# Kernel tuning notes

Measured on AMD Instinct MI355X. Metric: run time of the kernel, lower is better.

Reference implementation:

```python
import jax, jax.numpy as jnp
import numpy as np

SCALE = 1.0 / np.sqrt(128.0)  # 1/sqrt(head_size)
NEG = -1000000000.0


def setup_inputs() -> dict:
    key = jax.random.key(0)
    k1, k2, k3, k4 = jax.random.split(key, 4)
    B, H, S, D = 2, 16, 2048, 128
    q = jax.random.normal(k1, (B, H, S, D), dtype=jnp.float32)
    k = jax.random.normal(k2, (B, H, S, D), dtype=jnp.float32)
    v = jax.random.normal(k3, (B, H, S, D), dtype=jnp.float32)
    mask = jax.random.randint(k4, (B, S), 0, 2, dtype=jnp.int32)
    return {"q": q, "k": k, "v": v, "mask": mask}


def reference(q, k, v, mask):
    # scores: [B, H, Sq, Sk]
    scores = jnp.einsum("bhqd,bhkd->bhqk", q, k) * SCALE
    m = mask[:, None, None, :]  # [B,1,1,Sk], broadcast over heads and queries
    scores = jnp.where(m == 0, NEG, scores)
    weights = jax.nn.softmax(scores, axis=-1)
    out = jnp.einsum("bhqk,bhkd->bhqd", weights, v)
    return out
```

## Files before the change

kernel.cpp:

```cpp
#include <hip/hip_runtime.h>
#include <hip/hip_bf16.h>

typedef __attribute__((ext_vector_type(8))) short short8;
typedef __attribute__((ext_vector_type(4))) short short4v;
typedef __attribute__((ext_vector_type(4))) float floatx4;

#define NB 2
#define NH 16
#define NBH 32
#define SS 2048
#define DD 128
#define BQ 128
#define BK 32
#define KTILES (SS / BK)
#define SCALE 0.08838834764831845f
#define LOG2E 1.4426950408889634f
#define MAXB 12.0f
#define MASKED_BIAS -100000.0f

#define WC_VM4 0x0F74
#define WC_VM0 0x0F70
#define WC_ALL0 0x0070

__device__ __forceinline__ short f2bf(float f) {
  union { float f; unsigned u; } x; x.f = f;
  return (short)((x.u + 0x7FFFu + ((x.u >> 16) & 1u)) >> 16);
}

__device__ __forceinline__ void pack8(short8* dst, float a, float b, float c, float d,
                                      float e, float f, float g, float h) {
  union { __hip_bfloat162 h2[4]; short8 v; } u;
  u.h2[0] = __float22bfloat162_rn(make_float2(a, b));
  u.h2[1] = __float22bfloat162_rn(make_float2(c, d));
  u.h2[2] = __float22bfloat162_rn(make_float2(e, f));
  u.h2[3] = __float22bfloat162_rn(make_float2(g, h));
  *dst = u.v;
}

__device__ __forceinline__ void gload_lds16(const short* g, short* l) {
  __builtin_amdgcn_global_load_lds(
      (const __attribute__((address_space(1))) void*)(g),
      (__attribute__((address_space(3))) void*)(l), 16, 0, 0);
}

__global__ __launch_bounds__(256) void prep_kernel(const float* __restrict__ k,
                                                   const float* __restrict__ v,
                                                   short* __restrict__ kbf,
                                                   short* __restrict__ vtg) {
  __shared__ __align__(16) short Ts[DD * 64];
  const int kb = blockIdx.x, bh = blockIdx.y;
  const int tid = threadIdx.x;
  const size_t base = (size_t)bh * SS * DD + (size_t)(kb * 64) * DD;
  const float* kr = k + base;
  const float* vr = v + base;
  short* kw = kbf + base;

#pragma unroll
  for (int c = 0; c < 8; ++c) {
    int fi = c * 256 + tid;
    float4 a = ((const float4*)kr)[fi];
    short4v o;
    o[0] = f2bf(a.x); o[1] = f2bf(a.y); o[2] = f2bf(a.z); o[3] = f2bf(a.w);
    *(short4v*)(kw + (size_t)fi * 4) = o;
  }

  const int kg = tid & 15;
  const int dg0 = tid >> 4;
#pragma unroll
  for (int c = 0; c < 2; ++c) {
    int dg = dg0 + 16 * c;
    float rr[4][4];
#pragma unroll
    for (int r = 0; r < 4; ++r) {
      float4 a = ((const float4*)vr)[(kg * 4 + r) * 32 + dg];
      rr[r][0] = a.x; rr[r][1] = a.y; rr[r][2] = a.z; rr[r][3] = a.w;
    }
#pragma unroll
    for (int j = 0; j < 4; ++j) {
      int d = dg * 4 + j;
      short4v t;
      t[0] = f2bf(rr[0][j]); t[1] = f2bf(rr[1][j]);
      t[2] = f2bf(rr[2][j]); t[3] = f2bf(rr[3][j]);
      int si = d * 64 + (((kg * 8) ^ ((d & 15) << 3)) >> 1);
      *(short4v*)&Ts[si] = t;
    }
  }
  __syncthreads();

#pragma unroll
  for (int s = 0; s < 4; ++s) {
    int d = s * 32 + (tid >> 3);
    int c = tid & 7, kt2 = c >> 2, g = c & 3;
    int x = (d & 15) << 3;
    short4v lo = *(short4v*)&Ts[d * 64 + ((((kt2 * 8 + g) * 8) ^ x) >> 1)];
    short4v hi = *(short4v*)&Ts[d * 64 + ((((kt2 * 8 + g + 4) * 8) ^ x) >> 1)];
    short8 o;
#pragma unroll
    for (int r = 0; r < 4; ++r) { o[r] = lo[r]; o[4 + r] = hi[r]; }
    *(short8*)(vtg + ((size_t)(bh * DD + d)) * SS + (kb * 2 + kt2) * 32 + g * 8) = o;
  }
}

__global__ __launch_bounds__(256, 2) void fa_kernel(
    const float* __restrict__ q, const short* __restrict__ kbf,
    const short* __restrict__ vtg, const int* __restrict__ mask,
    float* __restrict__ out) {
  __shared__ __align__(16) short Ks[4][BK * DD];
  __shared__ __align__(16) short Vt[4][DD * BK];
  __shared__ float Bias[SS];

  const int tid = threadIdx.x;
  const int wave = tid >> 6;
  const int lane = tid & 63;
  const int l16 = lane & 15;
  const int quad = lane >> 4;

  const int lid = blockIdx.y * 16 + blockIdx.x;
  const int vid = (lid & 7) * 64 + (lid >> 3);
  const int bh = vid >> 4;
  const int q0 = (vid & 15) * BQ;
  const int b = bh >> 4;
  const int kt0off = ((bh >> 1) & 1) << 5;

  const size_t base = (size_t)bh * SS * DD;
  const float* qg = q + base;
  const short* kg = kbf + base;
  const short* vgb = vtg + (size_t)bh * DD * SS;
  const int* mg = mask + b * SS;
  const float c1 = SCALE * LOG2E, c2 = MAXB * LOG2E;

  short8 qf[2][4];
#pragma unroll
  for (int t = 0; t < 2; ++t) {
    const float* qp = qg + (size_t)(q0 + wave * 32 + t * 16 + l16) * DD;
#pragma unroll
    for (int dc = 0; dc < 4; ++dc) {
      float4 a = *(const float4*)(qp + dc * 32 + quad * 8);
      float4 bb = *(const float4*)(qp + dc * 32 + quad * 8 + 4);
      short8 tt;
      tt[0] = f2bf(a.x); tt[1] = f2bf(a.y); tt[2] = f2bf(a.z); tt[3] = f2bf(a.w);
      tt[4] = f2bf(bb.x); tt[5] = f2bf(bb.y); tt[6] = f2bf(bb.z); tt[7] = f2bf(bb.w);
      qf[t][dc] = tt;
    }
  }

  {
    int i0 = tid * 8;
    int4 m0 = *(const int4*)(mg + i0);
    int4 m1 = *(const int4*)(mg + i0 + 4);
    float4 f0, f1;
    f0.x = m0.x ? -c2 : MASKED_BIAS; f0.y = m0.y ? -c2 : MASKED_BIAS;
    f0.z = m0.z ? -c2 : MASKED_BIAS; f0.w = m0.w ? -c2 : MASKED_BIAS;
    f1.x = m1.x ? -c2 : MASKED_BIAS; f1.y = m1.y ? -c2 : MASKED_BIAS;
    f1.z = m1.z ? -c2 : MASKED_BIAS; f1.w = m1.w ? -c2 : MASKED_BIAS;
    *(float4*)&Bias[i0] = f0;
    *(float4*)&Bias[i0 + 4] = f1;
  }

  floatx4 Oacc[2][8];
#pragma unroll
  for (int t = 0; t < 2; ++t)
#pragma unroll
    for (int f = 0; f < 8; ++f) Oacc[t][f] = (floatx4){0.f, 0.f, 0.f, 0.f};
  float l_acc[2] = {0.f, 0.f};

  const short* kpg[2];
  const short* vpg[2];
  int kls[2], vls[2];
#pragma unroll
  for (int i = 0; i < 2; ++i) {
    int c = wave * 2 + i;
    int krow = c * 4 + (lane >> 4);
    kpg[i] = kg + (size_t)krow * DD + (((lane & 15) ^ (krow & 7)) * 8);
    int d = c * 16 + (lane >> 2);
    vpg[i] = vgb + (size_t)d * SS + (((lane & 3) ^ ((lane >> 3) & 3)) * 8);
    kls[i] = c * 512;
    vls[i] = c * 512;
  }

  int koff[2];
#pragma unroll
  for (int nt = 0; nt < 2; ++nt) koff[nt] = (nt * 16 + l16) * DD;
  const int ksw = l16 & 7;
  const int voff = l16 * 32 + ((quad ^ ((l16 >> 1) & 3)) * 8);

#pragma unroll
  for (int tt = 0; tt < 3; ++tt) {
    const int ktp = (kt0off + tt) & (KTILES - 1);
    const size_t kadv = (size_t)ktp * (BK * DD);
    const int vadv = ktp * BK;
#pragma unroll
    for (int i = 0; i < 2; ++i) {
      gload_lds16(kpg[i] + kadv, &Ks[tt][kls[i]]);
      gload_lds16(vpg[i] + vadv, &Vt[tt][vls[i]]);
    }
  }
  __builtin_amdgcn_s_waitcnt(WC_ALL0);
  __builtin_amdgcn_s_barrier();

  floatx4 sacc[2][2];
#pragma unroll
  for (int t = 0; t < 2; ++t)
#pragma unroll
    for (int nt = 0; nt < 2; ++nt) sacc[t][nt] = (floatx4){0.f, 0.f, 0.f, 0.f};
  {
    const short* ksb = &Ks[0][0];
    __builtin_amdgcn_s_setprio(1);
#pragma unroll
    for (int nt = 0; nt < 2; ++nt)
#pragma unroll
      for (int dc = 0; dc < 4; ++dc) {
        short8 kf = *(const short8*)(ksb + koff[nt] + (((dc * 4 + quad) ^ ksw) * 8));
        sacc[0][nt] = __builtin_amdgcn_mfma_f32_16x16x32_bf16(kf, qf[0][dc], sacc[0][nt], 0, 0, 0);
        sacc[1][nt] = __builtin_amdgcn_mfma_f32_16x16x32_bf16(kf, qf[1][dc], sacc[1][nt], 0, 0, 0);
      }
    __builtin_amdgcn_s_setprio(0);
  }

#pragma unroll 1
  for (int i = 0; i < KTILES - 1; ++i) {
    const int kt = (i + kt0off) & (KTILES - 1);
    if (i + 2 < KTILES) __builtin_amdgcn_s_waitcnt(WC_VM4);
    else                __builtin_amdgcn_s_waitcnt(WC_VM0);
    __builtin_amdgcn_s_barrier();

    if (i + 3 < KTILES) {
      const int ktp = (kt + 3) & (KTILES - 1);
      const int ib = (i + 3) & 3;
      const size_t kadv = (size_t)ktp * (BK * DD);
      const int vadv = ktp * BK;
#pragma unroll
      for (int c2 = 0; c2 < 2; ++c2) {
        gload_lds16(kpg[c2] + kadv, &Ks[ib][kls[c2]]);
        gload_lds16(vpg[c2] + vadv, &Vt[ib][vls[c2]]);
      }
    }

    float4 bb0 = *(const float4*)&Bias[kt * 32 + quad * 4];
    float4 bb1 = *(const float4*)&Bias[kt * 32 + 16 + quad * 4];

    short8 pb[2];
#pragma unroll
    for (int t = 0; t < 2; ++t) {
      float e0 = __builtin_amdgcn_exp2f(fmaf(sacc[t][0][0], c1, bb0.x));
      float e1 = __builtin_amdgcn_exp2f(fmaf(sacc[t][0][1], c1, bb0.y));
      float e2 = __builtin_amdgcn_exp2f(fmaf(sacc[t][0][2], c1, bb0.z));
      float e3 = __builtin_amdgcn_exp2f(fmaf(sacc[t][0][3], c1, bb0.w));
      float g0 = __builtin_amdgcn_exp2f(fmaf(sacc[t][1][0], c1, bb1.x));
      float g1 = __builtin_amdgcn_exp2f(fmaf(sacc[t][1][1], c1, bb1.y));
      float g2 = __builtin_amdgcn_exp2f(fmaf(sacc[t][1][2], c1, bb1.z));
      float g3 = __builtin_amdgcn_exp2f(fmaf(sacc[t][1][3], c1, bb1.w));
      l_acc[t] += ((e0 + e1) + (e2 + e3)) + ((g0 + g1) + (g2 + g3));
      pack8(&pb[t], e0, e1, e2, e3, g0, g1, g2, g3);
    }

    {
      const short* ksb = &Ks[(i + 1) & 3][0];
#pragma unroll
      for (int t = 0; t < 2; ++t)
#pragma unroll
        for (int nt = 0; nt < 2; ++nt) sacc[t][nt] = (floatx4){0.f, 0.f, 0.f, 0.f};
      __builtin_amdgcn_s_setprio(1);
#pragma unroll
      for (int nt = 0; nt < 2; ++nt)
#pragma unroll
        for (int dc = 0; dc < 4; ++dc) {
          short8 kf = *(const short8*)(ksb + koff[nt] + (((dc * 4 + quad) ^ ksw) * 8));
          sacc[0][nt] = __builtin_amdgcn_mfma_f32_16x16x32_bf16(kf, qf[0][dc], sacc[0][nt], 0, 0, 0);
          sacc[1][nt] = __builtin_amdgcn_mfma_f32_16x16x32_bf16(kf, qf[1][dc], sacc[1][nt], 0, 0, 0);
        }
      __builtin_amdgcn_s_setprio(0);
    }

    {
      const short* vsb = &Vt[i & 3][0];
      __builtin_amdgcn_s_setprio(1);
#pragma unroll
      for (int f = 0; f < 8; ++f) {
        short8 vv = *(const short8*)(vsb + f * 512 + voff);
        Oacc[0][f] = __builtin_amdgcn_mfma_f32_16x16x32_bf16(vv, pb[0], Oacc[0][f], 0, 0, 0);
        Oacc[1][f] = __builtin_amdgcn_mfma_f32_16x16x32_bf16(vv, pb[1], Oacc[1][f], 0, 0, 0);
      }
      __builtin_amdgcn_s_setprio(0);
    }
  }

  {
    const int kt = (KTILES - 1 + kt0off) & (KTILES - 1);
    float4 bb0 = *(const float4*)&Bias[kt * 32 + quad * 4];
    float4 bb1 = *(const float4*)&Bias[kt * 32 + 16 + quad * 4];
    short8 pb[2];
#pragma unroll
    for (int t = 0; t < 2; ++t) {
      float e0 = __builtin_amdgcn_exp2f(fmaf(sacc[t][0][0], c1, bb0.x));
      float e1 = __builtin_amdgcn_exp2f(fmaf(sacc[t][0][1], c1, bb0.y));
      float e2 = __builtin_amdgcn_exp2f(fmaf(sacc[t][0][2], c1, bb0.z));
      float e3 = __builtin_amdgcn_exp2f(fmaf(sacc[t][0][3], c1, bb0.w));
      float g0 = __builtin_amdgcn_exp2f(fmaf(sacc[t][1][0], c1, bb1.x));
      float g1 = __builtin_amdgcn_exp2f(fmaf(sacc[t][1][1], c1, bb1.y));
      float g2 = __builtin_amdgcn_exp2f(fmaf(sacc[t][1][2], c1, bb1.z));
      float g3 = __builtin_amdgcn_exp2f(fmaf(sacc[t][1][3], c1, bb1.w));
      l_acc[t] += ((e0 + e1) + (e2 + e3)) + ((g0 + g1) + (g2 + g3));
      pack8(&pb[t], e0, e1, e2, e3, g0, g1, g2, g3);
    }
    const short* vsb = &Vt[(KTILES - 1) & 3][0];
#pragma unroll
    for (int f = 0; f < 8; ++f) {
      short8 vv = *(const short8*)(vsb + f * 512 + voff);
      Oacc[0][f] = __builtin_amdgcn_mfma_f32_16x16x32_bf16(vv, pb[0], Oacc[0][f], 0, 0, 0);
      Oacc[1][f] = __builtin_amdgcn_mfma_f32_16x16x32_bf16(vv, pb[1], Oacc[1][f], 0, 0, 0);
    }
  }

  float* og = out + base;
#pragma unroll
  for (int t = 0; t < 2; ++t) {
    float s = l_acc[t];
    s += __shfl_xor(s, 16);
    s += __shfl_xor(s, 32);
    float inv = 1.0f / s;
    float* orow = og + (size_t)(q0 + wave * 32 + t * 16 + l16) * DD + quad * 4;
#pragma unroll
    for (int f = 0; f < 8; ++f) {
      float4 w;
      w.x = Oacc[t][f][0] * inv;
      w.y = Oacc[t][f][1] * inv;
      w.z = Oacc[t][f][2] * inv;
      w.w = Oacc[t][f][3] * inv;
      *(float4*)(orow + f * 16) = w;
    }
  }
}

extern "C" void kernel_launch(void* const* d_in, const int* in_sizes, int n_in,
                              void* d_out, int out_size, void* d_ws, size_t ws_size,
                              hipStream_t stream) {
  const float* q = (const float*)d_in[0];
  const float* k = (const float*)d_in[1];
  const float* v = (const float*)d_in[2];
  const int* mask = (const int*)d_in[3];
  float* out = (float*)d_out;

  short* kbf = (short*)d_ws;
  short* vtg = kbf + (size_t)NBH * SS * DD;

  prep_kernel<<<dim3(SS / 64, NBH), dim3(256), 0, stream>>>(k, v, kbf, vtg);
  fa_kernel<<<dim3(SS / BQ, NBH), dim3(256), 0, stream>>>(q, kbf, vtg, mask, out);
}
```

Measured before the change: 204.6 us.

## Software-pipeline LDS fragment loads into registers one tile ahead of MFMAs

K and V fragments are now loaded from LDS into registers one iteration ahead, so the QK^T and PV MFMAs use operands already in registers instead of waiting on LDS reads. The prologue now waits only for the first tile's loads (vmcnt 8) rather than draining all three. It also issues the fourth tile's prefetch early. The loop is re-indexed to start at 1. This costs extra VGPRs (kf and vv arrays), which could lower occupancy.

```diff
diff --git a/kernel.cpp b/kernel.cpp
--- a/kernel.cpp
+++ b/kernel.cpp
@@ -20,7 +20,7 @@
 
 #define WC_VM4 0x0F74
 #define WC_VM0 0x0F70
-#define WC_ALL0 0x0070
+#define WC_VM8_LGKM0 0x0078
 
 __device__ __forceinline__ short f2bf(float f) {
   union { float f; unsigned u; } x; x.f = f;
@@ -195,37 +195,70 @@
       gload_lds16(vpg[i] + vadv, &Vt[tt][vls[i]]);
     }
   }
-  __builtin_amdgcn_s_waitcnt(WC_ALL0);
+  __builtin_amdgcn_s_waitcnt(WC_VM8_LGKM0);
   __builtin_amdgcn_s_barrier();
 
-  floatx4 sacc[2][2];
-#pragma unroll
-  for (int t = 0; t < 2; ++t)
-#pragma unroll
-    for (int nt = 0; nt < 2; ++nt) sacc[t][nt] = (floatx4){0.f, 0.f, 0.f, 0.f};
+  short8 kf[2][4], vv[8];
   {
     const short* ksb = &Ks[0][0];
+#pragma unroll
+    for (int nt = 0; nt < 2; ++nt)
+#pragma unroll
+      for (int dc = 0; dc < 4; ++dc)
+        kf[nt][dc] = *(const short8*)(ksb + koff[nt] + (((dc * 4 + quad) ^ ksw) * 8));
+  }
+
+  floatx4 sacc[2][2];
+
+  {
+    __builtin_amdgcn_s_waitcnt(WC_VM4);
+    __builtin_amdgcn_s_barrier();
+    {
+      const int ktp = (kt0off + 3) & (KTILES - 1);
+      const size_t kadv = (size_t)ktp * (BK * DD);
+      const int vadv = ktp * BK;
+#pragma unroll
+      for (int c2 = 0; c2 < 2; ++c2) {
+        gload_lds16(kpg[c2] + kadv, &Ks[3][kls[c2]]);
+        gload_lds16(vpg[c2] + vadv, &Vt[3][vls[c2]]);
+      }
+    }
+#pragma unroll
+    for (int t = 0; t < 2; ++t)
+#pragma unroll
+      for (int nt = 0; nt < 2; ++nt) sacc[t][nt] = (floatx4){0.f, 0.f, 0.f, 0.f};
     __builtin_amdgcn_s_setprio(1);
 #pragma unroll
     for (int nt = 0; nt < 2; ++nt)
 #pragma unroll
       for (int dc = 0; dc < 4; ++dc) {
-        short8 kf = *(const short8*)(ksb + koff[nt] + (((dc * 4 + quad) ^ ksw) * 8));
-        sacc[0][nt] = __builtin_amdgcn_mfma_f32_16x16x32_bf16(kf, qf[0][dc], sacc[0][nt], 0, 0, 0);
-        sacc[1][nt] = __builtin_amdgcn_mfma_f32_16x16x32_bf16(kf, qf[1][dc], sacc[1][nt], 0, 0, 0);
+        sacc[0][nt] = __builtin_amdgcn_mfma_f32_16x16x32_bf16(kf[nt][dc], qf[0][dc], sacc[0][nt], 0, 0, 0);
+        sacc[1][nt] = __builtin_amdgcn_mfma_f32_16x16x32_bf16(kf[nt][dc], qf[1][dc], sacc[1][nt], 0, 0, 0);
       }
     __builtin_amdgcn_s_setprio(0);
+    {
+      const short* ksb = &Ks[1][0];
+#pragma unroll
+      for (int nt = 0; nt < 2; ++nt)
+#pragma unroll
+        for (int dc = 0; dc < 4; ++dc)
+          kf[nt][dc] = *(const short8*)(ksb + koff[nt] + (((dc * 4 + quad) ^ ksw) * 8));
+    }
+    {
+      const short* vsb = &Vt[0][0];
+#pragma unroll
+      for (int f = 0; f < 8; ++f) vv[f] = *(const short8*)(vsb + f * 512 + voff);
+    }
   }
 
 #pragma unroll 1
-  for (int i = 0; i < KTILES - 1; ++i) {
-    const int kt = (i + kt0off) & (KTILES - 1);
+  for (int i = 1; i < KTILES; ++i) {
     if (i + 2 < KTILES) __builtin_amdgcn_s_waitcnt(WC_VM4);
     else                __builtin_amdgcn_s_waitcnt(WC_VM0);
     __builtin_amdgcn_s_barrier();
 
     if (i + 3 < KTILES) {
-      const int ktp = (kt + 3) & (KTILES - 1);
+      const int ktp = (i + 3 + kt0off) & (KTILES - 1);
       const int ib = (i + 3) & 3;
       const size_t kadv = (size_t)ktp * (BK * DD);
       const int vadv = ktp * BK;
@@ -236,8 +269,9 @@
       }
     }
 
-    float4 bb0 = *(const float4*)&Bias[kt * 32 + quad * 4];
-    float4 bb1 = *(const float4*)&Bias[kt * 32 + 16 + quad * 4];
+    const int ktp = (i - 1 + kt0off) & (KTILES - 1);
+    float4 bb0 = *(const float4*)&Bias[ktp * 32 + quad * 4];
+    float4 bb1 = *(const float4*)&Bias[ktp * 32 + 16 + quad * 4];
 
     short8 pb[2];
 #pragma unroll
@@ -254,41 +288,48 @@
       pack8(&pb[t], e0, e1, e2, e3, g0, g1, g2, g3);
     }
 
-    {
+#pragma unroll
+    for (int t = 0; t < 2; ++t)
+#pragma unroll
+      for (int nt = 0; nt < 2; ++nt) sacc[t][nt] = (floatx4){0.f, 0.f, 0.f, 0.f};
+    __builtin_amdgcn_s_setprio(1);
+#pragma unroll
+    for (int nt = 0; nt < 2; ++nt)
+#pragma unroll
+      for (int dc = 0; dc < 4; ++dc) {
+        sacc[0][nt] = __builtin_amdgcn_mfma_f32_16x16x32_bf16(kf[nt][dc], qf[0][dc], sacc[0][nt], 0, 0, 0);
+        sacc[1][nt] = __builtin_amdgcn_mfma_f32_16x16x32_bf16(kf[nt][dc], qf[1][dc], sacc[1][nt], 0, 0, 0);
+      }
+    __builtin_amdgcn_s_setprio(0);
+
+    if (i + 1 < KTILES) {
       const short* ksb = &Ks[(i + 1) & 3][0];
 #pragma unroll
-      for (int t = 0; t < 2; ++t)
-#pragma unroll
-        for (int nt = 0; nt < 2; ++nt) sacc[t][nt] = (floatx4){0.f, 0.f, 0.f, 0.f};
-      __builtin_amdgcn_s_setprio(1);
-#pragma unroll
       for (int nt = 0; nt < 2; ++nt)
 #pragma unroll
-        for (int dc = 0; dc < 4; ++dc) {
-          short8 kf = *(const short8*)(ksb + koff[nt] + (((dc * 4 + quad) ^ ksw) * 8));
-          sacc[0][nt] = __builtin_amdgcn_mfma_f32_16x16x32_bf16(kf, qf[0][dc], sacc[0][nt], 0, 0, 0);
-          sacc[1][nt] = __builtin_amdgcn_mfma_f32_16x16x32_bf16(kf, qf[1][dc], sacc[1][nt], 0, 0, 0);
-        }
-      __builtin_amdgcn_s_setprio(0);
-    }
+        for (int dc = 0; dc < 4; ++dc)
+          kf[nt][dc] = *(const short8*)(ksb + koff[nt] + (((dc * 4 + quad) ^ ksw) * 8));
+    }
+
+    __builtin_amdgcn_s_setprio(1);
+#pragma unroll
+    for (int f = 0; f < 8; ++f) {
+      Oacc[0][f] = __builtin_amdgcn_mfma_f32_16x16x32_bf16(vv[f], pb[0], Oacc[0][f], 0, 0, 0);
+      Oacc[1][f] = __builtin_amdgcn_mfma_f32_16x16x32_bf16(vv[f], pb[1], Oacc[1][f], 0, 0, 0);
+    }
+    __builtin_amdgcn_s_setprio(0);
 
     {
       const short* vsb = &Vt[i & 3][0];
-      __builtin_amdgcn_s_setprio(1);
-#pragma unroll
-      for (int f = 0; f < 8; ++f) {
-        short8 vv = *(const short8*)(vsb + f * 512 + voff);
-        Oacc[0][f] = __builtin_amdgcn_mfma_f32_16x16x32_bf16(vv, pb[0], Oacc[0][f], 0, 0, 0);
-        Oacc[1][f] = __builtin_amdgcn_mfma_f32_16x16x32_bf16(vv, pb[1], Oacc[1][f], 0, 0, 0);
-      }
-      __builtin_amdgcn_s_setprio(0);
+#pragma unroll
+      for (int f = 0; f < 8; ++f) vv[f] = *(const short8*)(vsb + f * 512 + voff);
     }
   }
 
   {
-    const int kt = (KTILES - 1 + kt0off) & (KTILES - 1);
-    float4 bb0 = *(const float4*)&Bias[kt * 32 + quad * 4];
-    float4 bb1 = *(const float4*)&Bias[kt * 32 + 16 + quad * 4];
+    const int ktp = (KTILES - 1 + kt0off) & (KTILES - 1);
+    float4 bb0 = *(const float4*)&Bias[ktp * 32 + quad * 4];
+    float4 bb1 = *(const float4*)&Bias[ktp * 32 + 16 + quad * 4];
     short8 pb[2];
 #pragma unroll
     for (int t = 0; t < 2; ++t) {
@@ -303,12 +344,10 @@
       l_acc[t] += ((e0 + e1) + (e2 + e3)) + ((g0 + g1) + (g2 + g3));
       pack8(&pb[t], e0, e1, e2, e3, g0, g1, g2, g3);
     }
-    const short* vsb = &Vt[(KTILES - 1) & 3][0];
 #pragma unroll
     for (int f = 0; f < 8; ++f) {
-      short8 vv = *(const short8*)(vsb + f * 512 + voff);
-      Oacc[0][f] = __builtin_amdgcn_mfma_f32_16x16x32_bf16(vv, pb[0], Oacc[0][f], 0, 0, 0);
-      Oacc[1][f] = __builtin_amdgcn_mfma_f32_16x16x32_bf16(vv, pb[1], Oacc[1][f], 0, 0, 0);
+      Oacc[0][f] = __builtin_amdgcn_mfma_f32_16x16x32_bf16(vv[f], pb[0], Oacc[0][f], 0, 0, 0);
+      Oacc[1][f] = __builtin_amdgcn_mfma_f32_16x16x32_bf16(vv[f], pb[1], Oacc[1][f], 0, 0, 0);
     }
   }
 
```

Measured after the change: 206.9 us. No clear change (+1.1%).
